# Kernel tuning notes

Measured on AMD Instinct MI355X. Metric: run time of the kernel, lower is better.

## Reference

```python
import jax, jax.numpy as jnp
import numpy as np

N, D, E, EDGE_DIM, HID4 = 8192, 128, 262144, 50, 32


def setup_inputs() -> dict:
    key = jax.random.key(0)
    k = jax.random.split(key, 8)
    return {
        "mag": jax.random.uniform(k[0], (N, D), dtype=jnp.float32),
        "phase": jax.random.normal(k[1], (N, D), dtype=jnp.float32),
        "edge_index": jax.random.randint(k[2], (2, E), 0, N, dtype=jnp.int64),
        "rbf": jax.random.uniform(k[3], (E, EDGE_DIM), dtype=jnp.float32),
        "W1": jax.random.normal(k[4], (EDGE_DIM, HID4), dtype=jnp.float32) * 0.1,
        "b1": jnp.zeros((HID4,), dtype=jnp.float32),
        "W2": jax.random.normal(k[5], (HID4, 1), dtype=jnp.float32) * 0.1,
        "b2": jnp.zeros((1,), dtype=jnp.float32),
    }


def reference(mag, phase, edge_index, rbf, W1, b1, W2, b2):
    # score_ij = sum_d |z_i||z_j| cos(theta_i - theta_j) / sqrt(D)
    # cos(a-b) identity: = (mag*cos(phase)) @ (mag*cos(phase))^T + (mag*sin)@(mag*sin)^T
    scale = jnp.sqrt(jnp.asarray(mag.shape[-1], mag.dtype))
    a = mag * jnp.cos(phase)  # [N, D]
    b = mag * jnp.sin(phase)  # [N, D]
    scores = (a @ a.T + b @ b.T) / scale  # [N, N]
    # edge bias: Linear -> SiLU -> Linear -> scalar, scattered onto (i, j)
    h = jax.nn.silu(rbf @ W1 + b1)       # [E, HID4]
    bias = (h @ W2 + b2)[:, 0]           # [E]
    scores = scores.at[edge_index[0], edge_index[1]].add(bias)
    attn = jax.nn.softmax(scores, axis=1)  # softmax over keys j
    new_mag = attn @ mag
    new_phase = attn @ phase
    return new_mag, new_phase
```

## Files before the change

kernel.cpp:

```cpp
#include <hip/hip_runtime.h>
#include <hip/hip_bf16.h>

#define NN 8192
#define DD 128
#define DQK 256
#define EE 262144
#define EDGE_DIM 50
#define HID 32
#define CAP 96
#define SCALE 0.08838834764831845f
#define SCALE_LOG2E 0.12752455522410585f

using f32x4 = __attribute__((ext_vector_type(4))) float;
using f32x2 = __attribute__((ext_vector_type(2))) float;
using bf16x8 = __attribute__((ext_vector_type(8))) short;
using s16x4 = __attribute__((ext_vector_type(4))) short;

static __device__ __forceinline__ short f2b(float f) {
  __hip_bfloat16 h = __float2bfloat16(f);
  return __builtin_bit_cast(short, h);
}
static __device__ __forceinline__ float b2f(short s) {
  unsigned u = ((unsigned)(unsigned short)s) << 16;
  return __builtin_bit_cast(float, u);
}
static __device__ __forceinline__ void gll(const short* g, short* l) {
  __builtin_amdgcn_global_load_lds(
      (const __attribute__((address_space(1))) void*)g,
      (__attribute__((address_space(3))) void*)l, 16, 0, 0);
}

__global__ __launch_bounds__(256) void k1_mega(
    const float* __restrict__ mag, const float* __restrict__ phase,
    short* __restrict__ qkb, short* __restrict__ vtb, short* __restrict__ vb16,
    const float* __restrict__ rbf, const float* __restrict__ W1,
    const float* __restrict__ b1, const float* __restrict__ W2,
    const float* __restrict__ b2, const int* __restrict__ eidx,
    float* __restrict__ bias, int* __restrict__ cnt, int* __restrict__ slot) {
  __shared__ float tile[64][65];
  int b = blockIdx.x;
  int tid = threadIdx.x;
  if (b < 4096) {
    int t = b * 256 + tid;
    int n = t >> 7, d = t & 127;
    float m = mag[t], p = phase[t];
    float sn, cs;
    __sincosf(p, &sn, &cs);
    qkb[(size_t)n * DQK + d] = f2b(m * cs);
    qkb[(size_t)n * DQK + 128 + d] = f2b(m * sn);
    vb16[(size_t)n * DQK + d] = f2b(m);
    vb16[(size_t)n * DQK + 128 + d] = f2b(p);
    return;
  }
  if (b < 4608) {
    int r = b - 4096;
    int bn = r & 127, bd = (r >> 7) & 1, sel = r >> 8;
    const float* src = sel ? phase : mag;
#pragma unroll
    for (int rep = 0; rep < 16; ++rep) {
      int idx = rep * 256 + tid;
      int rr = idx >> 6, c = idx & 63;
      tile[rr][c] = src[(size_t)(bn * 64 + rr) * DD + bd * 64 + c];
    }
    __syncthreads();
#pragma unroll
    for (int rep = 0; rep < 16; ++rep) {
      int idx = rep * 256 + tid;
      int rr = idx >> 6, c = idx & 63;
      vtb[(size_t)(sel * 128 + bd * 64 + rr) * NN + bn * 64 + c] = f2b(tile[c][rr]);
    }
    return;
  }
  int e = (b - 4608) * 256 + tid;
  const float* rrow = rbf + (size_t)e * EDGE_DIM;
  f32x4 r4[12];
#pragma unroll
  for (int k = 0; k < 12; ++k) r4[k] = *reinterpret_cast<const f32x4*>(rrow + 4 * k);
  f32x2 rt2 = *reinterpret_cast<const f32x2*>(rrow + 48);
  float h[HID];
#pragma unroll
  for (int jj = 0; jj < HID; ++jj) h[jj] = b1[jj];
#pragma unroll
  for (int k = 0; k < 48; ++k) {
    float r = r4[k >> 2][k & 3];
#pragma unroll
    for (int jj = 0; jj < HID; ++jj) h[jj] += r * W1[k * HID + jj];
  }
#pragma unroll
  for (int jj = 0; jj < HID; ++jj)
    h[jj] += rt2.x * W1[48 * HID + jj] + rt2.y * W1[49 * HID + jj];
  float outv = b2[0];
#pragma unroll
  for (int jj = 0; jj < HID; ++jj) {
    float x = h[jj];
    outv += W2[jj] * (x / (1.0f + __expf(-x)));
  }
  bias[e] = outv;
  int i = eidx[e];
  int p = atomicAdd(&cnt[i], 1);
  if (p < CAP) slot[i * CAP + p] = e;
}

__global__ __launch_bounds__(64) void k2_merge(
    const int* __restrict__ eidx, const float* __restrict__ bias,
    const int* __restrict__ cntArr, const int* __restrict__ slot,
    unsigned* __restrict__ edgeJB, int* __restrict__ mcnt) {
  __shared__ int js[CAP];
  __shared__ float bs[CAP];
  int i = blockIdx.x;
  int lane = threadIdx.x;
  int cnt = cntArr[i];
  if (cnt > CAP) cnt = CAP;
  for (int p = lane; p < cnt; p += 64) {
    int e = slot[i * CAP + p];
    js[p] = eidx[EE + e];
    bs[p] = bias[e];
  }
  __syncthreads();
  for (int p = lane; p < cnt; p += 64) {
    int j = js[p];
    float bsum = bs[p];
    int keep = 1;
    for (int qq = 0; qq < cnt; ++qq) {
      if (qq == p || js[qq] != j) continue;
      if (qq < p) { keep = 0; break; }
      bsum += bs[qq];
    }
    unsigned v = keep ? (((unsigned)j << 16) |
                         (unsigned short)f2b(__expf(bsum)))
                      : 0xFFFF0000u;
    edgeJB[(size_t)i * CAP + p] = v;
  }
  if (lane == 0) mcnt[i] = cnt;
}

constexpr int TBM = 64;
constexpr int TBN = 128;

template <int NSPLIT>
__global__ __launch_bounds__(512, 4) void k5_flash(
    const short* __restrict__ qk,
    const short* __restrict__ vt,
    const unsigned* __restrict__ ejb,
    const int* __restrict__ mcnt,
    float* __restrict__ nump,
    float* __restrict__ denp) {
  constexpr int QCOLS = NN / NSPLIT;
  constexpr int NCHUNK = QCOLS / TBN;
  constexpr int GPQ = 8 / NSPLIT;
  __shared__ alignas(16) short Qs[TBM * 256];
  __shared__ alignas(16) short KV[2 * TBN * 64];
  __shared__ alignas(16) short Ps[TBM * 128];
  int b = blockIdx.x;
  int q = (b & 7) / GPQ;
  int rb = (b >> 3) * GPQ + (b & (GPQ - 1));
  int tid = threadIdx.x;
  int w = tid >> 6, lane = tid & 63;
  int wr = w >> 2, wc = w & 3;
  int l15 = lane & 15, quad = lane >> 4;
  int rsw = l15 & 7;
  int wbase = w * 64;
  int r0 = rb * TBM;
  int cbase = q * QCOLS;

#pragma unroll
  for (int p = 0; p < 4; ++p) {
    int idx = p * 512 + tid;
    int row = idx >> 5, gs = idx & 31;
    gll(qk + (size_t)(r0 + row) * DQK + ((gs ^ (row & 7)) * 8),
        &Qs[(p * 512 + wbase) * 8]);
  }

  int row8 = tid >> 3, sl0 = tid & 7;
  int mc = mcnt[r0 + row8];
  const unsigned* erow = ejb + (size_t)(r0 + row8) * CAP;
  unsigned myE[12];
#pragma unroll
  for (int u = 0; u < 12; ++u) {
    int t = sl0 + u * 8;
    myE[u] = (t < mc) ? erow[t] : 0xFFFF0000u;
  }
  float denAcc = 0.f;

  f32x4 o[2][4] = {};
  float den[2] = {0.f, 0.f};
  __syncthreads();

  for (int ch = 0; ch < NCHUNK; ++ch) {
    int c0 = cbase + ch * TBN;
#pragma unroll
    for (int p = 0; p < 2; ++p) {
      int idx = p * 512 + tid;
      int col = idx >> 3, gs = idx & 7;
      gll(qk + (size_t)(c0 + col) * DQK + ((gs ^ (col & 7)) * 8),
          &KV[(p * 512 + wbase) * 8]);
    }
    __syncthreads();
    f32x4 s[2][2] = {};
#pragma unroll
    for (int bk = 0; bk < 4; ++bk) {
      int buf = bk & 1;
      if (bk < 3) {
        int nb = buf ^ 1;
#pragma unroll
        for (int p = 0; p < 2; ++p) {
          int idx = p * 512 + tid;
          int col = idx >> 3, gs = idx & 7;
          gll(qk + (size_t)(c0 + col) * DQK + (bk + 1) * 64 + ((gs ^ (col & 7)) * 8),
              &KV[nb * 8192 + (p * 512 + wbase) * 8]);
        }
      }
#pragma unroll
      for (int ks = 0; ks < 2; ++ks) {
        int g = ks * 4 + quad;
        bf16x8 a[2], bb[2];
#pragma unroll
        for (int rt = 0; rt < 2; ++rt)
          a[rt] = *(const bf16x8*)&Qs[(wr * 32 + rt * 16 + l15) * 256 +
                                      ((bk * 8 + g) ^ rsw) * 8];
#pragma unroll
        for (int ct = 0; ct < 2; ++ct)
          bb[ct] = *(const bf16x8*)&KV[buf * 8192 + (wc * 32 + ct * 16 + l15) * 64 +
                                       (g ^ rsw) * 8];
#pragma unroll
        for (int rt = 0; rt < 2; ++rt)
#pragma unroll
          for (int ct = 0; ct < 2; ++ct)
            s[ct][rt] = __builtin_amdgcn_mfma_f32_16x16x32_bf16(bb[ct], a[rt],
                                                                s[ct][rt], 0, 0, 0);
      }
      __syncthreads();
    }
#pragma unroll
    for (int p = 0; p < 4; ++p) {
      int idx = p * 512 + tid;
      int feat = idx >> 3, gs = idx & 7;
      gll(vt + (size_t)feat * NN + c0 + ((gs ^ (feat & 7)) * 8),
          &KV[(p * 512 + wbase) * 8]);
    }
#pragma unroll
    for (int rt = 0; rt < 2; ++rt) {
      int row = wr * 32 + rt * 16 + l15;
#pragma unroll
      for (int ct = 0; ct < 2; ++ct) {
        s16x4 pk;
#pragma unroll
        for (int r = 0; r < 4; ++r) {
          float pv = exp2f(s[ct][rt][r] * SCALE_LOG2E);
          den[rt] += pv;
          pk[r] = f2b(pv);
        }
        int cg = wc * 4 + ct * 2 + (quad >> 1);
        *reinterpret_cast<s16x4*>(
            &Ps[row * 128 + ((cg ^ (row & 7)) * 8 + (quad & 1) * 4)]) = pk;
      }
    }
    __syncthreads();
#pragma unroll
    for (int u = 0; u < 12; ++u) {
      unsigned dj = (myE[u] >> 16) - (unsigned)c0;
      if (dj < (unsigned)TBN) {
        float eb = b2f((short)(myE[u] & 0xFFFFu));
        if (eb != 1.0f) {
          short* ps = &Ps[row8 * 128 + (((dj >> 3) ^ (row8 & 7)) * 8 + (int)(dj & 7))];
          float oldp = b2f(*ps);
          *ps = f2b(oldp * eb);
          denAcc += oldp * (eb - 1.0f);
        }
      }
    }
    __syncthreads();
#pragma unroll
    for (int jb = 0; jb < 2; ++jb) {
      if (jb == 1) {
        __syncthreads();
#pragma unroll
        for (int p = 0; p < 4; ++p) {
          int idx = p * 512 + tid;
          int feat = idx >> 3, gs = idx & 7;
          gll(vt + (size_t)feat * NN + c0 + 64 + ((gs ^ (feat & 7)) * 8),
              &KV[(p * 512 + wbase) * 8]);
        }
        __syncthreads();
      }
#pragma unroll
      for (int ks = 0; ks < 2; ++ks) {
        int g = ks * 4 + quad;
        bf16x8 pa[2], vb[4];
#pragma unroll
        for (int rt = 0; rt < 2; ++rt) {
          int row = wr * 32 + rt * 16 + l15;
          pa[rt] = *(const bf16x8*)&Ps[row * 128 +
                                       (((jb * 8 + g) ^ (row & 7)) * 8)];
        }
#pragma unroll
        for (int ft = 0; ft < 4; ++ft)
          vb[ft] = *(const bf16x8*)&KV[(wc * 64 + ft * 16 + l15) * 64 + (g ^ rsw) * 8];
#pragma unroll
        for (int rt = 0; rt < 2; ++rt)
#pragma unroll
          for (int ft = 0; ft < 4; ++ft)
            o[rt][ft] = __builtin_amdgcn_mfma_f32_16x16x32_bf16(pa[rt], vb[ft],
                                                                o[rt][ft], 0, 0, 0);
      }
    }
    __syncthreads();
  }
  float* npB = nump + (size_t)q * NN * DQK;
#pragma unroll
  for (int rt = 0; rt < 2; ++rt)
#pragma unroll
    for (int ft = 0; ft < 4; ++ft) {
      int row = r0 + wr * 32 + rt * 16 + quad * 4;
      int feat = wc * 64 + ft * 16 + l15;
#pragma unroll
      for (int r = 0; r < 4; ++r)
        npB[(size_t)(row + r) * DQK + feat] = o[rt][ft][r];
    }
  float* dl = reinterpret_cast<float*>(KV);
  float* corr = reinterpret_cast<float*>(KV) + 4 * TBM;
#pragma unroll
  for (int rt = 0; rt < 2; ++rt) {
    float d = den[rt];
    d += __shfl_xor(d, 16);
    d += __shfl_xor(d, 32);
    if (lane < 16) dl[wc * TBM + wr * 32 + rt * 16 + lane] = d;
  }
  denAcc += __shfl_xor(denAcc, 1);
  denAcc += __shfl_xor(denAcc, 2);
  denAcc += __shfl_xor(denAcc, 4);
  if (sl0 == 0) corr[row8] = denAcc;
  __syncthreads();
  if (tid < TBM) {
    float d = dl[0 * TBM + tid] + dl[1 * TBM + tid] + dl[2 * TBM + tid] +
              dl[3 * TBM + tid] + corr[tid];
    denp[q * NN + r0 + tid] = d;
  }
}

__global__ __launch_bounds__(64) void k6_norm(
    const float* __restrict__ nump, const float* __restrict__ denp,
    float* __restrict__ out, int nsplit) {
  int i = blockIdx.x;
  int lane = threadIdx.x;
  f32x4 a = {0.f, 0.f, 0.f, 0.f};
  float den = 0.f;
  for (int qq = 0; qq < nsplit; ++qq) {
    a += *reinterpret_cast<const f32x4*>(nump + ((size_t)qq * NN + i) * DQK + lane * 4);
    den += denp[qq * NN + i];
  }
  float inv = 1.0f / den;
  a *= inv;
  float* dst = (lane < 32) ? (out + (size_t)i * DD + lane * 4)
                           : (out + (size_t)NN * DD + (size_t)i * DD + lane * 4 - 128);
  *reinterpret_cast<f32x4*>(dst) = a;
}

constexpr size_t OFF_QK = 0;
constexpr size_t OFF_VT = (size_t)NN * DQK * 2;
constexpr size_t OFF_VB16 = OFF_VT + (size_t)DQK * NN * 2;
constexpr size_t OFF_BIAS = OFF_VB16 + (size_t)NN * DQK * 2;
constexpr size_t OFF_CNT = OFF_BIAS + (size_t)EE * 4;
constexpr size_t OFF_SLOT = OFF_CNT + (size_t)NN * 4;
constexpr size_t OFF_EJB = (OFF_SLOT + (size_t)NN * CAP * 4 + 255) & ~(size_t)255;
constexpr size_t OFF_MCNT = OFF_EJB + (size_t)NN * CAP * 4;
constexpr size_t OFF_NUMP = (OFF_MCNT + (size_t)NN * 4 + 255) & ~(size_t)255;
constexpr size_t WS_NEED4 = OFF_NUMP + 4ull * NN * DQK * 4 + 4ull * NN * 4;
constexpr size_t WS_NEED2 = OFF_NUMP + 2ull * NN * DQK * 4 + 2ull * NN * 4;

extern "C" void kernel_launch(void* const* d_in, const int* in_sizes, int n_in,
                              void* d_out, int out_size, void* d_ws, size_t ws_size,
                              hipStream_t stream) {
  const float* mag = (const float*)d_in[0];
  const float* phase = (const float*)d_in[1];
  const int* eidx = (const int*)d_in[2];
  const float* rbf = (const float*)d_in[3];
  const float* W1 = (const float*)d_in[4];
  const float* b1 = (const float*)d_in[5];
  const float* W2 = (const float*)d_in[6];
  const float* b2 = (const float*)d_in[7];
  float* out = (float*)d_out;
  char* ws = (char*)d_ws;
  if (ws_size < WS_NEED2) return;
  int nsplit = (ws_size >= WS_NEED4) ? 4 : 2;

  short* qkb = (short*)(ws + OFF_QK);
  short* vtb = (short*)(ws + OFF_VT);
  short* vb16 = (short*)(ws + OFF_VB16);
  float* bias = (float*)(ws + OFF_BIAS);
  int* cnt = (int*)(ws + OFF_CNT);
  int* slot = (int*)(ws + OFF_SLOT);
  unsigned* edgeJB = (unsigned*)(ws + OFF_EJB);
  int* mcnt = (int*)(ws + OFF_MCNT);
  float* nump = (float*)(ws + OFF_NUMP);
  float* denp = (float*)(ws + OFF_NUMP + (size_t)nsplit * NN * DQK * 4);

  hipMemsetAsync(cnt, 0, (size_t)NN * 4, stream);
  k1_mega<<<5632, 256, 0, stream>>>(mag, phase, qkb, vtb, vb16, rbf, W1, b1, W2,
                                    b2, eidx, bias, cnt, slot);
  k2_merge<<<NN, 64, 0, stream>>>(eidx, bias, cnt, slot, edgeJB, mcnt);
  if (nsplit == 4)
    k5_flash<4><<<(NN / TBM) * 4, 512, 0, stream>>>(qkb, vtb, edgeJB, mcnt, nump, denp);
  else
    k5_flash<2><<<(NN / TBM) * 2, 512, 0, stream>>>(qkb, vtb, edgeJB, mcnt, nump, denp);
  k6_norm<<<NN, 64, 0, stream>>>(nump, denp, out, nsplit);
}
```

Measured before the change: 266.5 us.

## Sort edge list per row and walk it with a cursor in flash kernel

The merge kernel now compacts the deduplicated edges of each row into sorted order by column and records per-quarter offsets. The flash kernel then has one thread per row walk a cursor through its sorted edges for each column chunk. Previously 512 threads held 12 edge registers each and tested all of them against every chunk. This cuts per-chunk edge checks and register use, at the cost of serialised per-row loops on only 64 threads plus global loads inside the chunk loop.

After: 259.6 us, median of 2. 1.03x faster.

```diff
diff --git a/kernel.cpp b/kernel.cpp
--- a/kernel.cpp
+++ b/kernel.cpp
@@ -104,9 +104,11 @@
 __global__ __launch_bounds__(64) void k2_merge(
     const int* __restrict__ eidx, const float* __restrict__ bias,
     const int* __restrict__ cntArr, const int* __restrict__ slot,
-    unsigned* __restrict__ edgeJB, int* __restrict__ mcnt) {
+    unsigned* __restrict__ edgeJB, int* __restrict__ qoff) {
   __shared__ int js[CAP];
-  __shared__ float bs[CAP];
+  __shared__ float bsv[CAP];
+  __shared__ float bsum_s[CAP];
+  __shared__ unsigned char keepf[CAP];
   int i = blockIdx.x;
   int lane = threadIdx.x;
   int cnt = cntArr[i];
@@ -114,24 +116,36 @@
   for (int p = lane; p < cnt; p += 64) {
     int e = slot[i * CAP + p];
     js[p] = eidx[EE + e];
-    bs[p] = bias[e];
+    bsv[p] = bias[e];
   }
   __syncthreads();
   for (int p = lane; p < cnt; p += 64) {
     int j = js[p];
-    float bsum = bs[p];
-    int keep = 1;
+    float bsum = bsv[p];
+    int kp = 1;
     for (int qq = 0; qq < cnt; ++qq) {
       if (qq == p || js[qq] != j) continue;
-      if (qq < p) { keep = 0; break; }
-      bsum += bs[qq];
-    }
-    unsigned v = keep ? (((unsigned)j << 16) |
-                         (unsigned short)f2b(__expf(bsum)))
-                      : 0xFFFF0000u;
-    edgeJB[(size_t)i * CAP + p] = v;
-  }
-  if (lane == 0) mcnt[i] = cnt;
+      if (qq < p) { kp = 0; break; }
+      bsum += bsv[qq];
+    }
+    keepf[p] = (unsigned char)kp;
+    bsum_s[p] = bsum;
+  }
+  __syncthreads();
+  for (int p = lane; p < cnt; p += 64) {
+    if (!keepf[p]) continue;
+    int j = js[p];
+    int r = 0;
+    for (int qq = 0; qq < cnt; ++qq) r += (keepf[qq] && js[qq] < j);
+    edgeJB[(size_t)i * CAP + r] =
+        (((unsigned)j) << 16) | (unsigned short)f2b(__expf(bsum_s[p]));
+  }
+  if (lane < 5) {
+    int bound = lane * 2048;
+    int c = 0;
+    for (int qq = 0; qq < cnt; ++qq) c += (keepf[qq] && js[qq] < bound);
+    qoff[i * 5 + lane] = c;
+  }
 }
 
 constexpr int TBM = 64;
@@ -142,7 +156,7 @@
     const short* __restrict__ qk,
     const short* __restrict__ vt,
     const unsigned* __restrict__ ejb,
-    const int* __restrict__ mcnt,
+    const int* __restrict__ qoff,
     float* __restrict__ nump,
     float* __restrict__ denp) {
   constexpr int QCOLS = NN / NSPLIT;
@@ -171,14 +185,14 @@
         &Qs[(p * 512 + wbase) * 8]);
   }
 
-  int row8 = tid >> 3, sl0 = tid & 7;
-  int mc = mcnt[r0 + row8];
-  const unsigned* erow = ejb + (size_t)(r0 + row8) * CAP;
-  unsigned myE[12];
-#pragma unroll
-  for (int u = 0; u < 12; ++u) {
-    int t = sl0 + u * 8;
-    myE[u] = (t < mc) ? erow[t] : 0xFFFF0000u;
+  const unsigned* erow = ejb + (size_t)(r0 + (tid & 63)) * CAP;
+  int cursor = 0, cend = 0;
+  unsigned nextE = 0xFFFFFFFFu;
+  if (tid < TBM) {
+    int qb = cbase >> 11;
+    cursor = qoff[(r0 + tid) * 5 + qb];
+    cend = qoff[(r0 + tid) * 5 + qb + (QCOLS >> 11)];
+    if (cursor < cend) nextE = erow[cursor];
   }
   float denAcc = 0.f;
 
@@ -256,17 +270,17 @@
       }
     }
     __syncthreads();
-#pragma unroll
-    for (int u = 0; u < 12; ++u) {
-      unsigned dj = (myE[u] >> 16) - (unsigned)c0;
-      if (dj < (unsigned)TBN) {
-        float eb = b2f((short)(myE[u] & 0xFFFFu));
-        if (eb != 1.0f) {
-          short* ps = &Ps[row8 * 128 + (((dj >> 3) ^ (row8 & 7)) * 8 + (int)(dj & 7))];
-          float oldp = b2f(*ps);
-          *ps = f2b(oldp * eb);
-          denAcc += oldp * (eb - 1.0f);
-        }
+    if (tid < TBM) {
+      unsigned limit = (unsigned)(c0 + TBN);
+      while ((nextE >> 16) < limit) {
+        unsigned dj = (nextE >> 16) - (unsigned)c0;
+        float eb = b2f((short)(nextE & 0xFFFFu));
+        short* ps = &Ps[tid * 128 + (((dj >> 3) ^ (tid & 7)) * 8 + (int)(dj & 7))];
+        float oldp = b2f(*ps);
+        *ps = f2b(oldp * eb);
+        denAcc += oldp * (eb - 1.0f);
+        ++cursor;
+        nextE = (cursor < cend) ? erow[cursor] : 0xFFFFFFFFu;
       }
     }
     __syncthreads();
@@ -318,7 +332,6 @@
         npB[(size_t)(row + r) * DQK + feat] = o[rt][ft][r];
     }
   float* dl = reinterpret_cast<float*>(KV);
-  float* corr = reinterpret_cast<float*>(KV) + 4 * TBM;
 #pragma unroll
   for (int rt = 0; rt < 2; ++rt) {
     float d = den[rt];
@@ -326,14 +339,10 @@
     d += __shfl_xor(d, 32);
     if (lane < 16) dl[wc * TBM + wr * 32 + rt * 16 + lane] = d;
   }
-  denAcc += __shfl_xor(denAcc, 1);
-  denAcc += __shfl_xor(denAcc, 2);
-  denAcc += __shfl_xor(denAcc, 4);
-  if (sl0 == 0) corr[row8] = denAcc;
   __syncthreads();
   if (tid < TBM) {
     float d = dl[0 * TBM + tid] + dl[1 * TBM + tid] + dl[2 * TBM + tid] +
-              dl[3 * TBM + tid] + corr[tid];
+              dl[3 * TBM + tid] + denAcc;
     denp[q * NN + r0 + tid] = d;
   }
 }
@@ -363,8 +372,8 @@
 constexpr size_t OFF_CNT = OFF_BIAS + (size_t)EE * 4;
 constexpr size_t OFF_SLOT = OFF_CNT + (size_t)NN * 4;
 constexpr size_t OFF_EJB = (OFF_SLOT + (size_t)NN * CAP * 4 + 255) & ~(size_t)255;
-constexpr size_t OFF_MCNT = OFF_EJB + (size_t)NN * CAP * 4;
-constexpr size_t OFF_NUMP = (OFF_MCNT + (size_t)NN * 4 + 255) & ~(size_t)255;
+constexpr size_t OFF_QOFF = OFF_EJB + (size_t)NN * CAP * 4;
+constexpr size_t OFF_NUMP = (OFF_QOFF + (size_t)NN * 5 * 4 + 255) & ~(size_t)255;
 constexpr size_t WS_NEED4 = OFF_NUMP + 4ull * NN * DQK * 4 + 4ull * NN * 4;
 constexpr size_t WS_NEED2 = OFF_NUMP + 2ull * NN * DQK * 4 + 2ull * NN * 4;
 
@@ -391,17 +400,17 @@
   int* cnt = (int*)(ws + OFF_CNT);
   int* slot = (int*)(ws + OFF_SLOT);
   unsigned* edgeJB = (unsigned*)(ws + OFF_EJB);
-  int* mcnt = (int*)(ws + OFF_MCNT);
+  int* qoff = (int*)(ws + OFF_QOFF);
   float* nump = (float*)(ws + OFF_NUMP);
   float* denp = (float*)(ws + OFF_NUMP + (size_t)nsplit * NN * DQK * 4);
 
   hipMemsetAsync(cnt, 0, (size_t)NN * 4, stream);
   k1_mega<<<5632, 256, 0, stream>>>(mag, phase, qkb, vtb, vb16, rbf, W1, b1, W2,
                                     b2, eidx, bias, cnt, slot);
-  k2_merge<<<NN, 64, 0, stream>>>(eidx, bias, cnt, slot, edgeJB, mcnt);
+  k2_merge<<<NN, 64, 0, stream>>>(eidx, bias, cnt, slot, edgeJB, qoff);
   if (nsplit == 4)
-    k5_flash<4><<<(NN / TBM) * 4, 512, 0, stream>>>(qkb, vtb, edgeJB, mcnt, nump, denp);
+    k5_flash<4><<<(NN / TBM) * 4, 512, 0, stream>>>(qkb, vtb, edgeJB, qoff, nump, denp);
   else
-    k5_flash<2><<<(NN / TBM) * 2, 512, 0, stream>>>(qkb, vtb, edgeJB, mcnt, nump, denp);
+    k5_flash<2><<<(NN / TBM) * 2, 512, 0, stream>>>(qkb, vtb, edgeJB, qoff, nump, denp);
   k6_norm<<<NN, 64, 0, stream>>>(nump, denp, out, nsplit);
 }
```
